# Optimization experiments

Hardware: AMD Instinct MI355X
Metric: run time of the kernel (lower is better)

## Reference

```python
import jax, jax.numpy as jnp
import numpy as np

NEG_INF = -9e15
ALPHA = 0.2  # LeakyReLU negative slope

N = 8192
D_IN = 512
D_OUT = 256


def setup_inputs() -> dict:
    key = jax.random.key(0)
    k1, k2, k3, k4, k5 = jax.random.split(key, 5)
    features = jax.random.normal(k1, (N, D_IN), dtype=jnp.float32)
    adjacency_matrix = jax.random.randint(k2, (N, N), 0, 2, dtype=jnp.int32)
    # learned params (torch Linear stores [out, in]; we use [in, out] layout)
    s_phi = 1.0 / np.sqrt(D_IN)
    W_phi = jax.random.uniform(k3, (D_IN, D_OUT), jnp.float32, -s_phi, s_phi)
    s_v = 1.0 / np.sqrt(D_OUT)
    w_mu = jax.random.uniform(k4, (D_OUT,), jnp.float32, -s_v, s_v)
    w_xi = jax.random.uniform(k5, (D_OUT,), jnp.float32, -s_v, s_v)
    return {"features": features, "adjacency_matrix": adjacency_matrix,
            "W_phi": W_phi, "w_mu": w_mu, "w_xi": w_xi}


def reference(features, adjacency_matrix, W_phi, w_mu, w_xi):
    h = features @ W_phi                                   # [N, d_out]
    mu = h @ w_mu                                          # [N]
    xi = h @ w_xi                                          # [N]
    e = mu[:, None] + xi[None, :]                          # [N, N] additive scores
    e = jnp.where(e >= 0, e, ALPHA * e)                    # LeakyReLU
    e = jnp.where(adjacency_matrix > 0, e, NEG_INF)        # mask non-edges
    a = jax.nn.softmax(e, axis=1)                          # row softmax (dropout p=0)
    out = a @ h                                            # weighted aggregation
    return jax.nn.elu(out)
```

## Files before the change

kernel.cpp:

```cpp
#include <hip/hip_runtime.h>
#include <cstdint>
#include <cstddef>


#define LOG2E 1.44269504f

typedef __attribute__((ext_vector_type(8))) short short8;
typedef __attribute__((ext_vector_type(4))) float floatx4;

using uint_as1 = __attribute__((address_space(1))) unsigned int;
using uint_as3 = __attribute__((address_space(3))) unsigned int;

__device__ __forceinline__ void gld_lds16(const void* g, void* l) {
  __builtin_amdgcn_global_load_lds((const uint_as1*)g, (uint_as3*)l, 16, 0, 0);
}

__device__ __forceinline__ unsigned short f2b(float f) {
  unsigned u = __float_as_uint(f);
  u += 0x7fffu + ((u >> 16) & 1u);
  return (unsigned short)(u >> 16);
}
__device__ __forceinline__ float b2f(short s) {
  return __uint_as_float(((unsigned)(unsigned short)s) << 16);
}

__global__ void k_bitmask(const int* __restrict__ adj, unsigned long long* __restrict__ bm) {
  int gw = (blockIdx.x * 256 + threadIdx.x) >> 6;
  int lane = threadIdx.x & 63;
  size_t w0 = (size_t)gw * 128;
  for (int r = 0; r < 128; r += 4) {
    size_t wd = w0 + r;
    int v0 = adj[(wd + 0) * 64 + lane];
    int v1 = adj[(wd + 1) * 64 + lane];
    int v2 = adj[(wd + 2) * 64 + lane];
    int v3 = adj[(wd + 3) * 64 + lane];
    unsigned long long m0 = __ballot(v0 != 0);
    unsigned long long m1 = __ballot(v1 != 0);
    unsigned long long m2 = __ballot(v2 != 0);
    unsigned long long m3 = __ballot(v3 != 0);
    if (lane == 0) {
      bm[wd] = m0; bm[wd + 1] = m1; bm[wd + 2] = m2; bm[wd + 3] = m3;
    }
  }
}

__global__ void k_cvt_features(const float* __restrict__ f, unsigned short* __restrict__ fb) {
  int tid = blockIdx.x * 256 + threadIdx.x;
  float4 v = ((const float4*)f)[tid];
  ushort4 o = {f2b(v.x), f2b(v.y), f2b(v.z), f2b(v.w)};
  *(ushort4*)&fb[tid * 4] = o;
}

__global__ void k_prep_wt(const float* __restrict__ w, unsigned short* __restrict__ wt) {
  int tid = blockIdx.x * 256 + threadIdx.x;
  int n = tid >> 9, k = tid & 511;
  wt[n * 512 + k] = f2b(w[k * 256 + n]);
}

__global__ void k_prep_p(const float* __restrict__ w, const float* __restrict__ wmu,
                         const float* __restrict__ wxi, float* __restrict__ pmu,
                         float* __restrict__ pxi) {
  int tid = blockIdx.x * 256 + threadIdx.x;
  int k = tid >> 2, seg = tid & 3;
  float sm = 0.f, sx = 0.f;
  int base = k * 256 + seg * 64;
#pragma unroll
  for (int c = 0; c < 64; c += 4) {
    float4 wv = *(const float4*)&w[base + c];
    float4 mv = *(const float4*)&wmu[seg * 64 + c];
    float4 xv = *(const float4*)&wxi[seg * 64 + c];
    sm += wv.x * mv.x + wv.y * mv.y + wv.z * mv.z + wv.w * mv.w;
    sx += wv.x * xv.x + wv.y * xv.y + wv.z * xv.z + wv.w * xv.w;
  }
  sm += __shfl_xor(sm, 1); sm += __shfl_xor(sm, 2);
  sx += __shfl_xor(sx, 1); sx += __shfl_xor(sx, 2);
  if (seg == 0) { pmu[k] = sm; pxi[k] = sx; }
}

__global__ void k_mu_xi(const unsigned short* __restrict__ fb, const float* __restrict__ pmu,
                        const float* __restrict__ pxi, float* __restrict__ Emu,
                        float* __restrict__ Fmu, float* __restrict__ Exi,
                        float* __restrict__ Fxi) {
  int w = threadIdx.x >> 6, l = threadIdx.x & 63;
  int i = blockIdx.x * 4 + w;
  short8 fv = *(const short8*)&fb[i * 512 + l * 8];
  float m = 0.f, x = 0.f;
#pragma unroll
  for (int c = 0; c < 8; ++c) {
    float fvf = b2f(fv[c]);
    m = fmaf(fvf, pmu[l * 8 + c], m);
    x = fmaf(fvf, pxi[l * 8 + c], x);
  }
#pragma unroll
  for (int off = 32; off > 0; off >>= 1) {
    m += __shfl_xor(m, off);
    x += __shfl_xor(x, off);
  }
  if (l == 0) {
    float ms = m * LOG2E, xs = x * LOG2E;
    Emu[i] = __builtin_amdgcn_exp2f(ms);
    Fmu[i] = __builtin_amdgcn_exp2f(0.2f * ms);
    Exi[i] = __builtin_amdgcn_exp2f(xs);
    Fxi[i] = __builtin_amdgcn_exp2f(0.2f * xs);
  }
}

__global__ __launch_bounds__(256, 2) void k_gemm1(const unsigned short* __restrict__ fb,
                                                  const unsigned short* __restrict__ wt,
                                                  unsigned short* __restrict__ ht) {
  __shared__ __align__(16) unsigned short As[64 * 64];
  __shared__ __align__(16) unsigned short Bs[128 * 64];
  int t = threadIdx.x, w = t >> 6, l = t & 63;
  int bm_ = blockIdx.x >> 1, bn = blockIdx.x & 1;
  int m0 = bm_ * 64, n0 = bn * 128;
  int lr = l >> 3, lg = l & 7, g = lg ^ lr;
  int kg = l >> 4, ln = l & 15;
  floatx4 zero = {0.f, 0.f, 0.f, 0.f};
  floatx4 acc[4][2];
#pragma unroll
  for (int mf = 0; mf < 4; ++mf)
#pragma unroll
    for (int nf = 0; nf < 2; ++nf) acc[mf][nf] = zero;

  for (int it = 0; it < 8; ++it) {
    int k0 = it * 64;
#pragma unroll
    for (int q = 0; q < 2; ++q) {
      int row = w * 16 + q * 8 + lr;
      const void* gp = fb + (size_t)(m0 + row) * 512 + k0 + g * 8;
      int lb = __builtin_amdgcn_readfirstlane((w * 16 + q * 8) * 64);
      gld_lds16(gp, &As[lb]);
    }
#pragma unroll
    for (int q = 0; q < 4; ++q) {
      int row = w * 32 + q * 8 + lr;
      const void* gp = wt + (size_t)(n0 + row) * 512 + k0 + g * 8;
      int lb = __builtin_amdgcn_readfirstlane((w * 32 + q * 8) * 64);
      gld_lds16(gp, &Bs[lb]);
    }
    __syncthreads();
#pragma unroll
    for (int ks = 0; ks < 2; ++ks) {
      int gg = ks * 4 + kg;
      int swz = (gg ^ (ln & 7)) * 8;
      short8 bfr[2];
#pragma unroll
      for (int nf = 0; nf < 2; ++nf)
        bfr[nf] = *(const short8*)&Bs[(w * 32 + nf * 16 + ln) * 64 + swz];
#pragma unroll
      for (int mf = 0; mf < 4; ++mf) {
        short8 afr = *(const short8*)&As[(mf * 16 + ln) * 64 + swz];
#pragma unroll
        for (int nf = 0; nf < 2; ++nf)
          acc[mf][nf] = __builtin_amdgcn_mfma_f32_16x16x32_bf16(afr, bfr[nf], acc[mf][nf], 0, 0, 0);
      }
    }
    __syncthreads();
  }
#pragma unroll
  for (int mf = 0; mf < 4; ++mf)
#pragma unroll
    for (int nf = 0; nf < 2; ++nf) {
      int ng = n0 + w * 32 + nf * 16 + ln;
      int mg = m0 + mf * 16 + kg * 4;
      ushort4 o = {f2b(acc[mf][nf][0]), f2b(acc[mf][nf][1]),
                   f2b(acc[mf][nf][2]), f2b(acc[mf][nf][3])};
      *(ushort4*)&ht[(size_t)ng * 8192 + mg] = o;
    }
}

__global__ __launch_bounds__(256, 1) void k_gatt2(const unsigned char* __restrict__ bm8,
                                                  const unsigned short* __restrict__ ht,
                                                  const float* __restrict__ Emu,
                                                  const float* __restrict__ Fmu,
                                                  const float* __restrict__ Exi,
                                                  const float* __restrict__ Fxi,
                                                  float* __restrict__ nump,
                                                  float* __restrict__ zpart) {
  __shared__ __align__(16) unsigned short Bs[256 * 256];
  __shared__ __align__(16) unsigned char BitS[256 * 32];
  __shared__ __align__(16) float ExiS[256];
  __shared__ __align__(16) float FxiS[256];

  int t = threadIdx.x, w = t >> 6, l = t & 63;
  int ln = l & 15, kg = l >> 4, kg8 = kg * 8;
  int wi = w >> 1, wn = w & 1;
  int jb = blockIdx.x & 7, ig = blockIdx.x >> 3;
  int i0 = ig * 256;
  int jw0 = jb * 1024;

  float EM[8], FM[8];
#pragma unroll
  for (int mf = 0; mf < 8; ++mf) {
    int i = i0 + wi * 128 + mf * 16 + ln;
    EM[mf] = Emu[i];
    FM[mf] = Fmu[i];
  }

  floatx4 zero = {0.f, 0.f, 0.f, 0.f};
  floatx4 acc[8][8];
#pragma unroll
  for (int mf = 0; mf < 8; ++mf)
#pragma unroll
    for (int nf = 0; nf < 8; ++nf) acc[mf][nf] = zero;
  floatx4 accz[8];
#pragma unroll
  for (int mf = 0; mf < 8; ++mf) accz[mf] = zero;

  short8 ones;
#pragma unroll
  for (int e = 0; e < 8; ++e) ones[e] = (short)0x3F80;

  for (int win = 0; win < 4; ++win) {
    int jc = jw0 + win * 256;
    __syncthreads();
#pragma unroll
    for (int q = 0; q < 32; ++q) {
      int r0 = w * 64 + q * 2;
      int row = r0 + (l >> 5);
      int g = (l & 31) ^ (row & 31);
      const void* gp = ht + (size_t)row * 8192 + jc + g * 8;
      int lb = __builtin_amdgcn_readfirstlane(r0 * 256);
      gld_lds16(gp, &Bs[lb]);
    }
#pragma unroll
    for (int q2 = 0; q2 < 2; ++q2) {
      int r0 = w * 64 + q2 * 32;
      int row = r0 + (l >> 1);
      const void* gp = bm8 + (size_t)(i0 + row) * 1024 + jb * 128 + win * 32 + (l & 1) * 16;
      int lb = __builtin_amdgcn_readfirstlane(r0 * 32);
      gld_lds16(gp, &BitS[lb]);
    }
    if (w == 2) gld_lds16(Exi + jc + l * 4, &ExiS[0]);
    if (w == 3) gld_lds16(Fxi + jc + l * 4, &FxiS[0]);
    __syncthreads();

#pragma unroll
    for (int ks = 0; ks < 8; ++ks) {
      int gran = ks * 4 + kg;
      float4 e0 = *(const float4*)&ExiS[gran * 8];
      float4 e1 = *(const float4*)&ExiS[gran * 8 + 4];
      float4 f0 = *(const float4*)&FxiS[gran * 8];
      float4 f1 = *(const float4*)&FxiS[gran * 8 + 4];
      float ex[8] = {e0.x, e0.y, e0.z, e0.w, e1.x, e1.y, e1.z, e1.w};
      float fx[8] = {f0.x, f0.y, f0.z, f0.w, f1.x, f1.y, f1.z, f1.w};
      short8 bfv[8];
#pragma unroll
      for (int nf = 0; nf < 8; ++nf) {
        int n = wn * 128 + nf * 16 + ln;
        bfv[nf] = *(const short8*)&Bs[n * 256 + ((gran ^ (n & 31)) * 8)];
      }
#pragma unroll
      for (int mf = 0; mf < 8; ++mf) {
        unsigned bits = BitS[(wi * 128 + mf * 16 + ln) * 32 + gran];
        float A = EM[mf], F = FM[mf];
        float vv[8];
#pragma unroll
        for (int e = 0; e < 8; ++e) {
          float m = fmaxf(A * ex[e], F * fx[e]);
          vv[e] = (bits & (1u << e)) ? m : 0.f;
        }
        union { uint4 u; short8 s; } cv;
        cv.u.x = (__float_as_uint(vv[1]) & 0xFFFF0000u) | (__float_as_uint(vv[0]) >> 16);
        cv.u.y = (__float_as_uint(vv[3]) & 0xFFFF0000u) | (__float_as_uint(vv[2]) >> 16);
        cv.u.z = (__float_as_uint(vv[5]) & 0xFFFF0000u) | (__float_as_uint(vv[4]) >> 16);
        cv.u.w = (__float_as_uint(vv[7]) & 0xFFFF0000u) | (__float_as_uint(vv[6]) >> 16);
        short8 af = cv.s;
        accz[mf] = __builtin_amdgcn_mfma_f32_16x16x32_bf16(af, ones, accz[mf], 0, 0, 0);
#pragma unroll
        for (int nf = 0; nf < 8; ++nf)
          acc[mf][nf] = __builtin_amdgcn_mfma_f32_16x16x32_bf16(af, bfv[nf], acc[mf][nf], 0, 0, 0);
      }
    }
  }

  float* np = nump + (size_t)jb * (8192 * 256);
#pragma unroll
  for (int mf = 0; mf < 8; ++mf) {
    int rowb = i0 + wi * 128 + mf * 16 + kg * 4;
#pragma unroll
    for (int r = 0; r < 4; ++r) {
      float* rp = np + (size_t)(rowb + r) * 256 + wn * 128;
#pragma unroll
      for (int nf = 0; nf < 8; ++nf)
        rp[nf * 16 + ln] = acc[mf][nf][r];
    }
    if (wn == 0 && ln == 0) {
#pragma unroll
      for (int r = 0; r < 4; ++r)
        zpart[jb * 8192 + rowb + r] = accz[mf][r];
    }
  }
}

__global__ void k_final(const float* __restrict__ nump, const float* __restrict__ zpart,
                        float* __restrict__ out) {
  int tid = blockIdx.x * 256 + threadIdx.x;
  int i = tid >> 6;
  float z = 0.f;
#pragma unroll
  for (int p = 0; p < 8; ++p) z += zpart[p * 8192 + i];
  float zi = 1.0f / z;
  float4 v = {0.f, 0.f, 0.f, 0.f};
#pragma unroll
  for (int p = 0; p < 8; ++p) {
    float4 s = *(const float4*)&nump[(size_t)p * (8192 * 256) + tid * 4];
    v.x += s.x; v.y += s.y; v.z += s.z; v.w += s.w;
  }
  v.x *= zi; v.y *= zi; v.z *= zi; v.w *= zi;
  v.x = (v.x > 0.f) ? v.x : (__builtin_amdgcn_exp2f(v.x * LOG2E) - 1.f);
  v.y = (v.y > 0.f) ? v.y : (__builtin_amdgcn_exp2f(v.y * LOG2E) - 1.f);
  v.z = (v.z > 0.f) ? v.z : (__builtin_amdgcn_exp2f(v.z * LOG2E) - 1.f);
  v.w = (v.w > 0.f) ? v.w : (__builtin_amdgcn_exp2f(v.w * LOG2E) - 1.f);
  *(float4*)&out[tid * 4] = v;
}

extern "C" void kernel_launch(void* const* d_in, const int* in_sizes, int n_in,
                              void* d_out, int out_size, void* d_ws, size_t ws_size,
                              hipStream_t stream) {
  const float* features = (const float*)d_in[0];
  const int* adjm = (const int*)d_in[1];
  const float* W_phi = (const float*)d_in[2];
  const float* w_mu = (const float*)d_in[3];
  const float* w_xi = (const float*)d_in[4];
  float* out = (float*)d_out;

  char* ws = (char*)d_ws;
  unsigned short* fb  = (unsigned short*)(ws + 0);
  unsigned short* ht  = (unsigned short*)(ws + 8388608);
  unsigned short* wt  = (unsigned short*)(ws + 12582912);
  float* pmu = (float*)(ws + 12845056);
  float* pxi = (float*)(ws + 12847104);
  float* Emu = (float*)(ws + 12849152);
  float* Fmu = (float*)(ws + 12881920);
  float* Exi = (float*)(ws + 12914688);
  float* Fxi = (float*)(ws + 12947456);
  unsigned char* bmask = (unsigned char*)(ws + 13631488);
  float* zpart = (float*)(ws + 22020096);
  float* nump  = (float*)(ws + 25165824);

  k_bitmask<<<2048, 256, 0, stream>>>(adjm, (unsigned long long*)bmask);
  k_cvt_features<<<4096, 256, 0, stream>>>(features, fb);
  k_prep_wt<<<512, 256, 0, stream>>>(W_phi, wt);
  k_prep_p<<<8, 256, 0, stream>>>(W_phi, w_mu, w_xi, pmu, pxi);
  k_mu_xi<<<2048, 256, 0, stream>>>(fb, pmu, pxi, Emu, Fmu, Exi, Fxi);
  k_gemm1<<<256, 256, 0, stream>>>(fb, wt, ht);
  k_gatt2<<<256, 256, 0, stream>>>(bmask, ht, Emu, Fmu, Exi, Fxi, nump, zpart);
  k_final<<<2048, 256, 0, stream>>>(nump, zpart, out);
}
```

Baseline: 555.5 us.

## Double-buffer attention kernel, move softmax denominator into bitmask pass

The main attention-aggregation kernel is rebuilt with 512 threads, 128-row tiles, a 2048-column split and double-buffered LDS staging of h and mask tiles, so global loads overlap MFMA work. The row-sum denominator is no longer computed with an extra ones-MFMA per tile. It is now accumulated in fp32 inside the bitmask kernel, which reads the adjacency matrix anyway. This removes one MFMA per row fragment, cuts partial-output slices from 8 to 4, and changes rounding from bf16 truncation to round-to-nearest. The cost is a different occupancy and register profile, and a bitmask kernel that must now run after the mu/xi kernel.

```diff
diff --git a/kernel.cpp b/kernel.cpp
--- a/kernel.cpp
+++ b/kernel.cpp
@@ -24,24 +24,40 @@
   return __uint_as_float(((unsigned)(unsigned short)s) << 16);
 }
 
-__global__ void k_bitmask(const int* __restrict__ adj, unsigned long long* __restrict__ bm) {
+__global__ void k_bitmaskz(const int* __restrict__ adj,
+                           const float* __restrict__ Emu, const float* __restrict__ Fmu,
+                           const float* __restrict__ Exi, const float* __restrict__ Fxi,
+                           unsigned long long* __restrict__ bm, float* __restrict__ zbuf) {
   int gw = (blockIdx.x * 256 + threadIdx.x) >> 6;
   int lane = threadIdx.x & 63;
+  float EM = Emu[gw], FM = Fmu[gw];
   size_t w0 = (size_t)gw * 128;
+  float z = 0.f;
   for (int r = 0; r < 128; r += 4) {
     size_t wd = w0 + r;
     int v0 = adj[(wd + 0) * 64 + lane];
     int v1 = adj[(wd + 1) * 64 + lane];
     int v2 = adj[(wd + 2) * 64 + lane];
     int v3 = adj[(wd + 3) * 64 + lane];
+    float e0 = Exi[(r + 0) * 64 + lane], f0 = Fxi[(r + 0) * 64 + lane];
+    float e1 = Exi[(r + 1) * 64 + lane], f1 = Fxi[(r + 1) * 64 + lane];
+    float e2 = Exi[(r + 2) * 64 + lane], f2 = Fxi[(r + 2) * 64 + lane];
+    float e3 = Exi[(r + 3) * 64 + lane], f3 = Fxi[(r + 3) * 64 + lane];
     unsigned long long m0 = __ballot(v0 != 0);
     unsigned long long m1 = __ballot(v1 != 0);
     unsigned long long m2 = __ballot(v2 != 0);
     unsigned long long m3 = __ballot(v3 != 0);
+    z += (v0 != 0) ? fmaxf(EM * e0, FM * f0) : 0.f;
+    z += (v1 != 0) ? fmaxf(EM * e1, FM * f1) : 0.f;
+    z += (v2 != 0) ? fmaxf(EM * e2, FM * f2) : 0.f;
+    z += (v3 != 0) ? fmaxf(EM * e3, FM * f3) : 0.f;
     if (lane == 0) {
       bm[wd] = m0; bm[wd + 1] = m1; bm[wd + 2] = m2; bm[wd + 3] = m3;
     }
   }
+#pragma unroll
+  for (int off = 32; off > 0; off >>= 1) z += __shfl_xor(z, off);
+  if (lane == 0) zbuf[gw] = z;
 }
 
 __global__ void k_cvt_features(const float* __restrict__ f, unsigned short* __restrict__ fb) {
@@ -169,115 +185,114 @@
     }
 }
 
-__global__ __launch_bounds__(256, 1) void k_gatt2(const unsigned char* __restrict__ bm8,
+__global__ __launch_bounds__(512, 2) void k_gatt3(const unsigned char* __restrict__ bm8,
                                                   const unsigned short* __restrict__ ht,
                                                   const float* __restrict__ Emu,
                                                   const float* __restrict__ Fmu,
                                                   const float* __restrict__ Exi,
                                                   const float* __restrict__ Fxi,
-                                                  float* __restrict__ nump,
-                                                  float* __restrict__ zpart) {
-  __shared__ __align__(16) unsigned short Bs[256 * 256];
-  __shared__ __align__(16) unsigned char BitS[256 * 32];
-  __shared__ __align__(16) float ExiS[256];
-  __shared__ __align__(16) float FxiS[256];
+                                                  float* __restrict__ nump) {
+  __shared__ __align__(16) unsigned short Bs[2][256 * 128];
+  __shared__ __align__(16) unsigned char BitS[2][128 * 16];
+  __shared__ __align__(16) float EfE[2048];
+  __shared__ __align__(16) float EfF[2048];
 
   int t = threadIdx.x, w = t >> 6, l = t & 63;
-  int ln = l & 15, kg = l >> 4, kg8 = kg * 8;
+  int ln = l & 15, kg = l >> 4;
   int wi = w >> 1, wn = w & 1;
-  int jb = blockIdx.x & 7, ig = blockIdx.x >> 3;
-  int i0 = ig * 256;
-  int jw0 = jb * 1024;
-
-  float EM[8], FM[8];
-#pragma unroll
-  for (int mf = 0; mf < 8; ++mf) {
-    int i = i0 + wi * 128 + mf * 16 + ln;
+  int jb = blockIdx.x & 3, ig = blockIdx.x >> 2;
+  int i0 = ig * 128;
+  int jc0 = jb * 2048;
+
+  {
+    float4 e = *(const float4*)&Exi[jc0 + t * 4];
+    float4 f = *(const float4*)&Fxi[jc0 + t * 4];
+    *(float4*)&EfE[t * 4] = e;
+    *(float4*)&EfF[t * 4] = f;
+  }
+
+  float EM[2], FM[2];
+#pragma unroll
+  for (int mf = 0; mf < 2; ++mf) {
+    int i = i0 + wi * 32 + mf * 16 + ln;
     EM[mf] = Emu[i];
     FM[mf] = Fmu[i];
   }
 
   floatx4 zero = {0.f, 0.f, 0.f, 0.f};
-  floatx4 acc[8][8];
-#pragma unroll
-  for (int mf = 0; mf < 8; ++mf)
+  floatx4 acc[2][8];
+#pragma unroll
+  for (int mf = 0; mf < 2; ++mf)
 #pragma unroll
     for (int nf = 0; nf < 8; ++nf) acc[mf][nf] = zero;
-  floatx4 accz[8];
-#pragma unroll
-  for (int mf = 0; mf < 8; ++mf) accz[mf] = zero;
-
-  short8 ones;
-#pragma unroll
-  for (int e = 0; e < 8; ++e) ones[e] = (short)0x3F80;
-
-  for (int win = 0; win < 4; ++win) {
-    int jc = jw0 + win * 256;
-    __syncthreads();
-#pragma unroll
-    for (int q = 0; q < 32; ++q) {
-      int r0 = w * 64 + q * 2;
-      int row = r0 + (l >> 5);
-      int g = (l & 31) ^ (row & 31);
-      const void* gp = ht + (size_t)row * 8192 + jc + g * 8;
-      int lb = __builtin_amdgcn_readfirstlane(r0 * 256);
-      gld_lds16(gp, &Bs[lb]);
-    }
-#pragma unroll
-    for (int q2 = 0; q2 < 2; ++q2) {
-      int r0 = w * 64 + q2 * 32;
-      int row = r0 + (l >> 1);
-      const void* gp = bm8 + (size_t)(i0 + row) * 1024 + jb * 128 + win * 32 + (l & 1) * 16;
-      int lb = __builtin_amdgcn_readfirstlane(r0 * 32);
-      gld_lds16(gp, &BitS[lb]);
-    }
-    if (w == 2) gld_lds16(Exi + jc + l * 4, &ExiS[0]);
-    if (w == 3) gld_lds16(Fxi + jc + l * 4, &FxiS[0]);
-    __syncthreads();
-
-#pragma unroll
-    for (int ks = 0; ks < 8; ++ks) {
-      int gran = ks * 4 + kg;
-      float4 e0 = *(const float4*)&ExiS[gran * 8];
-      float4 e1 = *(const float4*)&ExiS[gran * 8 + 4];
-      float4 f0 = *(const float4*)&FxiS[gran * 8];
-      float4 f1 = *(const float4*)&FxiS[gran * 8 + 4];
+
+#define STAGE_HW(hw_, nb_)                                                    \
+  {                                                                           \
+    int j0_ = jc0 + (hw_) * 128;                                              \
+    _Pragma("unroll")                                                         \
+    for (int q = 0; q < 8; ++q) {                                             \
+      int r0 = w * 32 + q * 4;                                                \
+      int row = r0 + (l >> 4);                                                \
+      int g = (l & 15) ^ (row & 15);                                          \
+      const void* gp = ht + (size_t)row * 8192 + j0_ + g * 8;                 \
+      int lb = __builtin_amdgcn_readfirstlane(r0 * 128);                      \
+      gld_lds16(gp, &Bs[nb_][lb]);                                            \
+    }                                                                         \
+    if (w < 2) {                                                              \
+      int row = w * 64 + l;                                                   \
+      const void* gp = bm8 + (size_t)(i0 + row) * 1024 + (j0_ >> 3);          \
+      int lb = __builtin_amdgcn_readfirstlane(w * 64 * 16);                   \
+      gld_lds16(gp, &BitS[nb_][lb]);                                          \
+    }                                                                         \
+  }
+
+  STAGE_HW(0, 0);
+  __syncthreads();
+
+  for (int hw = 0; hw < 16; ++hw) {
+    int nb = hw & 1;
+    if (hw < 15) STAGE_HW(hw + 1, nb ^ 1);
+#pragma unroll
+    for (int ksl = 0; ksl < 4; ++ksl) {
+      int gran = ksl * 4 + kg;
+      int jl = hw * 128 + gran * 8;
+      float4 e0 = *(const float4*)&EfE[jl];
+      float4 e1 = *(const float4*)&EfE[jl + 4];
+      float4 f0 = *(const float4*)&EfF[jl];
+      float4 f1 = *(const float4*)&EfF[jl + 4];
       float ex[8] = {e0.x, e0.y, e0.z, e0.w, e1.x, e1.y, e1.z, e1.w};
       float fx[8] = {f0.x, f0.y, f0.z, f0.w, f1.x, f1.y, f1.z, f1.w};
       short8 bfv[8];
 #pragma unroll
       for (int nf = 0; nf < 8; ++nf) {
         int n = wn * 128 + nf * 16 + ln;
-        bfv[nf] = *(const short8*)&Bs[n * 256 + ((gran ^ (n & 31)) * 8)];
+        bfv[nf] = *(const short8*)&Bs[nb][n * 128 + ((gran ^ (n & 15)) * 8)];
       }
 #pragma unroll
-      for (int mf = 0; mf < 8; ++mf) {
-        unsigned bits = BitS[(wi * 128 + mf * 16 + ln) * 32 + gran];
+      for (int mf = 0; mf < 2; ++mf) {
+        int row = wi * 32 + mf * 16 + ln;
+        unsigned bw = *(const unsigned*)&BitS[nb][row * 16 + ksl * 4];
+        unsigned bits = (bw >> (kg * 8)) & 0xffu;
         float A = EM[mf], F = FM[mf];
-        float vv[8];
+        short8 af;
 #pragma unroll
         for (int e = 0; e < 8; ++e) {
           float m = fmaxf(A * ex[e], F * fx[e]);
-          vv[e] = (bits & (1u << e)) ? m : 0.f;
+          m = (bits & (1u << e)) ? m : 0.f;
+          af[e] = (short)f2b(m);
         }
-        union { uint4 u; short8 s; } cv;
-        cv.u.x = (__float_as_uint(vv[1]) & 0xFFFF0000u) | (__float_as_uint(vv[0]) >> 16);
-        cv.u.y = (__float_as_uint(vv[3]) & 0xFFFF0000u) | (__float_as_uint(vv[2]) >> 16);
-        cv.u.z = (__float_as_uint(vv[5]) & 0xFFFF0000u) | (__float_as_uint(vv[4]) >> 16);
-        cv.u.w = (__float_as_uint(vv[7]) & 0xFFFF0000u) | (__float_as_uint(vv[6]) >> 16);
-        short8 af = cv.s;
-        accz[mf] = __builtin_amdgcn_mfma_f32_16x16x32_bf16(af, ones, accz[mf], 0, 0, 0);
 #pragma unroll
         for (int nf = 0; nf < 8; ++nf)
           acc[mf][nf] = __builtin_amdgcn_mfma_f32_16x16x32_bf16(af, bfv[nf], acc[mf][nf], 0, 0, 0);
       }
     }
+    __syncthreads();
   }
 
   float* np = nump + (size_t)jb * (8192 * 256);
 #pragma unroll
-  for (int mf = 0; mf < 8; ++mf) {
-    int rowb = i0 + wi * 128 + mf * 16 + kg * 4;
+  for (int mf = 0; mf < 2; ++mf) {
+    int rowb = i0 + wi * 32 + mf * 16 + kg * 4;
 #pragma unroll
     for (int r = 0; r < 4; ++r) {
       float* rp = np + (size_t)(rowb + r) * 256 + wn * 128;
@@ -285,25 +300,18 @@
       for (int nf = 0; nf < 8; ++nf)
         rp[nf * 16 + ln] = acc[mf][nf][r];
     }
-    if (wn == 0 && ln == 0) {
-#pragma unroll
-      for (int r = 0; r < 4; ++r)
-        zpart[jb * 8192 + rowb + r] = accz[mf][r];
-    }
-  }
-}
-
-__global__ void k_final(const float* __restrict__ nump, const float* __restrict__ zpart,
+  }
+#undef STAGE_HW
+}
+
+__global__ void k_final(const float* __restrict__ nump, const float* __restrict__ zbuf,
                         float* __restrict__ out) {
   int tid = blockIdx.x * 256 + threadIdx.x;
   int i = tid >> 6;
-  float z = 0.f;
-#pragma unroll
-  for (int p = 0; p < 8; ++p) z += zpart[p * 8192 + i];
-  float zi = 1.0f / z;
+  float zi = 1.0f / zbuf[i];
   float4 v = {0.f, 0.f, 0.f, 0.f};
 #pragma unroll
-  for (int p = 0; p < 8; ++p) {
+  for (int p = 0; p < 4; ++p) {
     float4 s = *(const float4*)&nump[(size_t)p * (8192 * 256) + tid * 4];
     v.x += s.x; v.y += s.y; v.z += s.z; v.w += s.w;
   }
@@ -335,16 +343,17 @@
   float* Fmu = (float*)(ws + 12881920);
   float* Exi = (float*)(ws + 12914688);
   float* Fxi = (float*)(ws + 12947456);
+  float* zbuf = (float*)(ws + 12980224);
   unsigned char* bmask = (unsigned char*)(ws + 13631488);
-  float* zpart = (float*)(ws + 22020096);
-  float* nump  = (float*)(ws + 25165824);
-
-  k_bitmask<<<2048, 256, 0, stream>>>(adjm, (unsigned long long*)bmask);
+  float* nump = (float*)(ws + 25165824);
+
   k_cvt_features<<<4096, 256, 0, stream>>>(features, fb);
   k_prep_wt<<<512, 256, 0, stream>>>(W_phi, wt);
   k_prep_p<<<8, 256, 0, stream>>>(W_phi, w_mu, w_xi, pmu, pxi);
   k_mu_xi<<<2048, 256, 0, stream>>>(fb, pmu, pxi, Emu, Fmu, Exi, Fxi);
   k_gemm1<<<256, 256, 0, stream>>>(fb, wt, ht);
-  k_gatt2<<<256, 256, 0, stream>>>(bmask, ht, Emu, Fmu, Exi, Fxi, nump, zpart);
-  k_final<<<2048, 256, 0, stream>>>(nump, zpart, out);
-}
+  k_bitmaskz<<<2048, 256, 0, stream>>>(adjm, Emu, Fmu, Exi, Fxi,
+                                       (unsigned long long*)bmask, zbuf);
+  k_gatt3<<<256, 512, 0, stream>>>(bmask, ht, Emu, Fmu, Exi, Fxi, nump);
+  k_final<<<2048, 256, 0, stream>>>(nump, zbuf, out);
+}
```

New measurement: 472.6 us. 1.18x faster.

## Retile attention kernel to smaller tiles with double-buffered LDS and register bitmasks

Applied to the files above, without the earlier changes.

Replaces the 256x256-tile attention kernel with a 128x128 tile over 1024 blocks, launch bounds allowing three blocks per CU. Uses double-buffered 64-wide K slices of ht loaded asynchronously into LDS, so loads overlap MFMA compute. Reads mask bits straight from global into registers and packs Exi/Fxi into one bf16 pair in LDS. The cost is that each block now computes the score/mask A-fragments for only half of the output columns, so that elementwise work is duplicated across two blocks. Smaller tiles also lower per-block reuse.

```diff
diff --git a/kernel.cpp b/kernel.cpp
--- a/kernel.cpp
+++ b/kernel.cpp
@@ -169,7 +169,7 @@
     }
 }
 
-__global__ __launch_bounds__(256, 1) void k_gatt2(const unsigned char* __restrict__ bm8,
+__global__ __launch_bounds__(256, 3) void k_gatt4(const unsigned long long* __restrict__ bm64,
                                                   const unsigned short* __restrict__ ht,
                                                   const float* __restrict__ Emu,
                                                   const float* __restrict__ Fmu,
@@ -177,112 +177,134 @@
                                                   const float* __restrict__ Fxi,
                                                   float* __restrict__ nump,
                                                   float* __restrict__ zpart) {
-  __shared__ __align__(16) unsigned short Bs[256 * 256];
-  __shared__ __align__(16) unsigned char BitS[256 * 32];
-  __shared__ __align__(16) float ExiS[256];
-  __shared__ __align__(16) float FxiS[256];
+  __shared__ __align__(16) unsigned short Bs[2][128 * 64];
+  __shared__ __align__(16) unsigned int EfP[1024];
 
   int t = threadIdx.x, w = t >> 6, l = t & 63;
-  int ln = l & 15, kg = l >> 4, kg8 = kg * 8;
+  int ln = l & 15, kg = l >> 4;
   int wi = w >> 1, wn = w & 1;
-  int jb = blockIdx.x & 7, ig = blockIdx.x >> 3;
-  int i0 = ig * 256;
-  int jw0 = jb * 1024;
-
-  float EM[8], FM[8];
-#pragma unroll
-  for (int mf = 0; mf < 8; ++mf) {
-    int i = i0 + wi * 128 + mf * 16 + ln;
+  int b = blockIdx.x;
+  int jb = b & 7, nb = (b >> 3) & 1, ig = b >> 4;
+  int i0 = ig * 128, n0 = nb * 128, jc0 = jb * 1024;
+
+  {
+    float4 e = *(const float4*)&Exi[jc0 + t * 4];
+    float4 f = *(const float4*)&Fxi[jc0 + t * 4];
+    uint4 p;
+    p.x = (__float_as_uint(f.x) & 0xffff0000u) | (__float_as_uint(e.x) >> 16);
+    p.y = (__float_as_uint(f.y) & 0xffff0000u) | (__float_as_uint(e.y) >> 16);
+    p.z = (__float_as_uint(f.z) & 0xffff0000u) | (__float_as_uint(e.z) >> 16);
+    p.w = (__float_as_uint(f.w) & 0xffff0000u) | (__float_as_uint(e.w) >> 16);
+    *(uint4*)&EfP[t * 4] = p;
+  }
+
+  float EM[4], FM[4];
+#pragma unroll
+  for (int mf = 0; mf < 4; ++mf) {
+    int i = i0 + wi * 64 + mf * 16 + ln;
     EM[mf] = Emu[i];
     FM[mf] = Fmu[i];
   }
 
   floatx4 zero = {0.f, 0.f, 0.f, 0.f};
-  floatx4 acc[8][8];
-#pragma unroll
-  for (int mf = 0; mf < 8; ++mf)
-#pragma unroll
-    for (int nf = 0; nf < 8; ++nf) acc[mf][nf] = zero;
-  floatx4 accz[8];
-#pragma unroll
-  for (int mf = 0; mf < 8; ++mf) accz[mf] = zero;
+  floatx4 acc[4][4];
+#pragma unroll
+  for (int mf = 0; mf < 4; ++mf)
+#pragma unroll
+    for (int nf = 0; nf < 4; ++nf) acc[mf][nf] = zero;
+  floatx4 accz[4];
+#pragma unroll
+  for (int mf = 0; mf < 4; ++mf) accz[mf] = zero;
 
   short8 ones;
 #pragma unroll
   for (int e = 0; e < 8; ++e) ones[e] = (short)0x3F80;
 
-  for (int win = 0; win < 4; ++win) {
-    int jc = jw0 + win * 256;
-    __syncthreads();
-#pragma unroll
-    for (int q = 0; q < 32; ++q) {
-      int r0 = w * 64 + q * 2;
-      int row = r0 + (l >> 5);
-      int g = (l & 31) ^ (row & 31);
-      const void* gp = ht + (size_t)row * 8192 + jc + g * 8;
-      int lb = __builtin_amdgcn_readfirstlane(r0 * 256);
-      gld_lds16(gp, &Bs[lb]);
-    }
-#pragma unroll
-    for (int q2 = 0; q2 < 2; ++q2) {
-      int r0 = w * 64 + q2 * 32;
-      int row = r0 + (l >> 1);
-      const void* gp = bm8 + (size_t)(i0 + row) * 1024 + jb * 128 + win * 32 + (l & 1) * 16;
-      int lb = __builtin_amdgcn_readfirstlane(r0 * 32);
-      gld_lds16(gp, &BitS[lb]);
-    }
-    if (w == 2) gld_lds16(Exi + jc + l * 4, &ExiS[0]);
-    if (w == 3) gld_lds16(Fxi + jc + l * 4, &FxiS[0]);
-    __syncthreads();
-
-#pragma unroll
-    for (int ks = 0; ks < 8; ++ks) {
-      int gran = ks * 4 + kg;
-      float4 e0 = *(const float4*)&ExiS[gran * 8];
-      float4 e1 = *(const float4*)&ExiS[gran * 8 + 4];
-      float4 f0 = *(const float4*)&FxiS[gran * 8];
-      float4 f1 = *(const float4*)&FxiS[gran * 8 + 4];
-      float ex[8] = {e0.x, e0.y, e0.z, e0.w, e1.x, e1.y, e1.z, e1.w};
-      float fx[8] = {f0.x, f0.y, f0.z, f0.w, f1.x, f1.y, f1.z, f1.w};
-      short8 bfv[8];
-#pragma unroll
-      for (int nf = 0; nf < 8; ++nf) {
-        int n = wn * 128 + nf * 16 + ln;
-        bfv[nf] = *(const short8*)&Bs[n * 256 + ((gran ^ (n & 31)) * 8)];
+  const unsigned long long* bp[4];
+#pragma unroll
+  for (int mf = 0; mf < 4; ++mf)
+    bp[mf] = bm64 + (size_t)(i0 + wi * 64 + mf * 16 + ln) * 128 + jb * 16;
+
+#define STAGE(hw_, b_)                                                        \
+  {                                                                           \
+    int j0_ = jc0 + (hw_) * 64;                                               \
+    _Pragma("unroll")                                                         \
+    for (int q = 0; q < 4; ++q) {                                             \
+      int r0 = w * 32 + q * 8;                                                \
+      int row = r0 + (l >> 3);                                                \
+      int g = (l & 7) ^ (row & 7);                                            \
+      const void* gp = ht + (size_t)(n0 + row) * 8192 + j0_ + g * 8;          \
+      int lb = __builtin_amdgcn_readfirstlane((b_) * (128 * 64) + r0 * 64);   \
+      gld_lds16(gp, &Bs[0][lb]);                                              \
+    }                                                                         \
+  }
+
+  unsigned long long bc[4], bnx[4];
+#pragma unroll
+  for (int mf = 0; mf < 4; ++mf) bc[mf] = bp[mf][0];
+  STAGE(0, 0);
+  __syncthreads();
+
+  for (int hw = 0; hw < 16; ++hw) {
+    int buf = hw & 1;
+    if (hw < 15) {
+      STAGE(hw + 1, buf ^ 1);
+#pragma unroll
+      for (int mf = 0; mf < 4; ++mf) bnx[mf] = bp[mf][hw + 1];
+    }
+#pragma unroll
+    for (int ksl = 0; ksl < 2; ++ksl) {
+      int gran = ksl * 4 + kg;
+      int jl = hw * 64 + gran * 8;
+      uint4 p0 = *(const uint4*)&EfP[jl];
+      uint4 p1 = *(const uint4*)&EfP[jl + 4];
+      unsigned pe[8] = {p0.x, p0.y, p0.z, p0.w, p1.x, p1.y, p1.z, p1.w};
+      short8 bfv[4];
+#pragma unroll
+      for (int nf = 0; nf < 4; ++nf) {
+        int n = wn * 64 + nf * 16 + ln;
+        bfv[nf] = *(const short8*)&Bs[buf][n * 64 + ((gran ^ (n & 7)) * 8)];
       }
 #pragma unroll
-      for (int mf = 0; mf < 8; ++mf) {
-        unsigned bits = BitS[(wi * 128 + mf * 16 + ln) * 32 + gran];
+      for (int mf = 0; mf < 4; ++mf) {
+        unsigned bits = (unsigned)(bc[mf] >> (ksl * 32));
+        bits = (bits >> (kg * 8)) & 0xffu;
         float A = EM[mf], F = FM[mf];
         float vv[8];
 #pragma unroll
         for (int e = 0; e < 8; ++e) {
-          float m = fmaxf(A * ex[e], F * fx[e]);
+          float Ef = __uint_as_float(pe[e] << 16);
+          float Ff = __uint_as_float(pe[e] & 0xffff0000u);
+          float m = fmaxf(A * Ef, F * Ff);
           vv[e] = (bits & (1u << e)) ? m : 0.f;
         }
         union { uint4 u; short8 s; } cv;
-        cv.u.x = (__float_as_uint(vv[1]) & 0xFFFF0000u) | (__float_as_uint(vv[0]) >> 16);
-        cv.u.y = (__float_as_uint(vv[3]) & 0xFFFF0000u) | (__float_as_uint(vv[2]) >> 16);
-        cv.u.z = (__float_as_uint(vv[5]) & 0xFFFF0000u) | (__float_as_uint(vv[4]) >> 16);
-        cv.u.w = (__float_as_uint(vv[7]) & 0xFFFF0000u) | (__float_as_uint(vv[6]) >> 16);
+        cv.u.x = (__float_as_uint(vv[1]) & 0xffff0000u) | (__float_as_uint(vv[0]) >> 16);
+        cv.u.y = (__float_as_uint(vv[3]) & 0xffff0000u) | (__float_as_uint(vv[2]) >> 16);
+        cv.u.z = (__float_as_uint(vv[5]) & 0xffff0000u) | (__float_as_uint(vv[4]) >> 16);
+        cv.u.w = (__float_as_uint(vv[7]) & 0xffff0000u) | (__float_as_uint(vv[6]) >> 16);
         short8 af = cv.s;
         accz[mf] = __builtin_amdgcn_mfma_f32_16x16x32_bf16(af, ones, accz[mf], 0, 0, 0);
 #pragma unroll
-        for (int nf = 0; nf < 8; ++nf)
+        for (int nf = 0; nf < 4; ++nf)
           acc[mf][nf] = __builtin_amdgcn_mfma_f32_16x16x32_bf16(af, bfv[nf], acc[mf][nf], 0, 0, 0);
       }
     }
-  }
+    __syncthreads();
+#pragma unroll
+    for (int mf = 0; mf < 4; ++mf) bc[mf] = bnx[mf];
+  }
+#undef STAGE
 
   float* np = nump + (size_t)jb * (8192 * 256);
 #pragma unroll
-  for (int mf = 0; mf < 8; ++mf) {
-    int rowb = i0 + wi * 128 + mf * 16 + kg * 4;
+  for (int mf = 0; mf < 4; ++mf) {
+    int rowb = i0 + wi * 64 + mf * 16 + kg * 4;
 #pragma unroll
     for (int r = 0; r < 4; ++r) {
-      float* rp = np + (size_t)(rowb + r) * 256 + wn * 128;
-#pragma unroll
-      for (int nf = 0; nf < 8; ++nf)
+      float* rp = np + (size_t)(rowb + r) * 256 + n0 + wn * 64;
+#pragma unroll
+      for (int nf = 0; nf < 4; ++nf)
         rp[nf * 16 + ln] = acc[mf][nf][r];
     }
     if (wn == 0 && ln == 0) {
@@ -335,16 +357,16 @@
   float* Fmu = (float*)(ws + 12881920);
   float* Exi = (float*)(ws + 12914688);
   float* Fxi = (float*)(ws + 12947456);
-  unsigned char* bmask = (unsigned char*)(ws + 13631488);
+  unsigned long long* bmask = (unsigned long long*)(ws + 13631488);
   float* zpart = (float*)(ws + 22020096);
   float* nump  = (float*)(ws + 25165824);
 
-  k_bitmask<<<2048, 256, 0, stream>>>(adjm, (unsigned long long*)bmask);
   k_cvt_features<<<4096, 256, 0, stream>>>(features, fb);
   k_prep_wt<<<512, 256, 0, stream>>>(W_phi, wt);
   k_prep_p<<<8, 256, 0, stream>>>(W_phi, w_mu, w_xi, pmu, pxi);
   k_mu_xi<<<2048, 256, 0, stream>>>(fb, pmu, pxi, Emu, Fmu, Exi, Fxi);
   k_gemm1<<<256, 256, 0, stream>>>(fb, wt, ht);
-  k_gatt2<<<256, 256, 0, stream>>>(bmask, ht, Emu, Fmu, Exi, Fxi, nump, zpart);
+  k_bitmask<<<2048, 256, 0, stream>>>(adjm, bmask);
+  k_gatt4<<<1024, 256, 0, stream>>>(bmask, ht, Emu, Fmu, Exi, Fxi, nump, zpart);
   k_final<<<2048, 256, 0, stream>>>(nump, zpart, out);
 }
```

Result: faster. 501.3 us (-9.8%).
